# Kernel tuning notes

Measured on AMD Instinct MI355X. Metric: run time of the kernel, lower is better.

## Reference

```python
import jax, jax.numpy as jnp
import numpy as np

C_IN = 128
C_QK = C_IN // 8


def setup_inputs() -> dict:
    key = jax.random.key(0)
    kx, kq, kk, kv = jax.random.split(key, 4)
    x = jax.random.normal(kx, (8, C_IN, 64, 64), dtype=jnp.float32)
    # 1x1 conv weights, stored as (c_out, c_in); fan-in scaled init
    s = 1.0 / np.sqrt(C_IN)
    Wq = jax.random.normal(kq, (C_QK, C_IN), dtype=jnp.float32) * s
    Wk = jax.random.normal(kk, (C_QK, C_IN), dtype=jnp.float32) * s
    Wv = jax.random.normal(kv, (C_IN, C_IN), dtype=jnp.float32) * s
    gamma = jnp.ones((1,), dtype=jnp.float32) * 0.5  # nonzero so residual branch matters
    return {"x": x, "Wq": Wq, "Wk": Wk, "Wv": Wv, "gamma": gamma}


def reference(x, Wq, Wk, Wv, gamma):
    b, c, h, w = x.shape
    xt = rearr = x.reshape(b, c, h * w)            # b c n
    q = jnp.einsum('oc,bcn->bno', Wq, xt)          # b n c//8
    k = jnp.einsum('oc,bcn->bon', Wk, xt)          # b c//8 n
    v = jnp.einsum('oc,bcn->bno', Wv, xt)          # b n c
    energy = jnp.einsum('bno,bom->bnm', q, k)      # b n n (no scale, per source)
    attn = jax.nn.softmax(energy, axis=-1)
    out = jnp.einsum('bnm,bmc->bnc', attn, v)      # b n c
    out = out.transpose(0, 2, 1).reshape(b, c, h, w)
    return x + gamma[0] * out
```

## Files before the change

### kernel.cpp

```cpp
#include <hip/hip_runtime.h>
#include <hip/hip_bf16.h>


typedef __bf16 bf16x8 __attribute__((ext_vector_type(8)));
typedef __bf16 bf16x4 __attribute__((ext_vector_type(4)));
typedef float  f32x16 __attribute__((ext_vector_type(16)));

static constexpr int Bb = 8, Cc = 128, Nn = 4096, CQ = 16;

__device__ __forceinline__ f32x16 mfma32(bf16x8 a, bf16x8 b, f32x16 c) {
    return __builtin_amdgcn_mfma_f32_32x32x16_bf16(a, b, c, 0, 0, 0);
}
struct HL { __bf16 h, l; };
__device__ __forceinline__ HL hilo(float f) {
    HL r;
    r.h = (__bf16)f;
    r.l = (__bf16)(f - (float)r.h);
    return r;
}

__global__ __launch_bounds__(384) void qkv_kernel(
    const float* __restrict__ x, const float* __restrict__ Wq,
    const float* __restrict__ Wk, const float* __restrict__ Wv,
    __bf16* __restrict__ qw, __bf16* __restrict__ kw, __bf16* __restrict__ vw)
{
    const int b = blockIdx.y, tb = blockIdx.x, n0 = tb * 64, t = threadIdx.x;
    const int wave = t >> 6, lane = t & 63, lr = lane & 31, lq = lane >> 5;

    __shared__ __bf16 xh[64][136], xl[64][136];
    __shared__ __bf16 sc[4][32][40];

    if (t < 256) {
        const int n = lane, ci0 = (t >> 6) * 32;
        #pragma unroll
        for (int g = 0; g < 4; ++g) {
            float v[8];
            #pragma unroll
            for (int k = 0; k < 8; ++k)
                v[k] = x[((size_t)(b * Cc + ci0 + g * 8 + k)) * Nn + n0 + n];
            bf16x8 h8, l8;
            #pragma unroll
            for (int k = 0; k < 8; ++k) { HL z = hilo(v[k]); h8[k] = z.h; l8[k] = z.l; }
            *(bf16x8*)&xh[n][ci0 + g * 8] = h8;
            *(bf16x8*)&xl[n][ci0 + g * 8] = l8;
        }
    }
    __syncthreads();

    if (wave < 2) {
        const int nh = wave;
        const float* wrow = (lr < 16) ? (Wq + (size_t)lr * Cc)
                                      : (Wk + (size_t)(lr - 16) * Cc);
        f32x16 acc = {};
        #pragma unroll
        for (int ks = 0; ks < 8; ++ks) {
            float4 w0 = *(const float4*)(wrow + ks * 16 + lq * 8);
            float4 w1 = *(const float4*)(wrow + ks * 16 + lq * 8 + 4);
            bf16x8 ah, al;
            HL z;
            z = hilo(w0.x); ah[0] = z.h; al[0] = z.l;
            z = hilo(w0.y); ah[1] = z.h; al[1] = z.l;
            z = hilo(w0.z); ah[2] = z.h; al[2] = z.l;
            z = hilo(w0.w); ah[3] = z.h; al[3] = z.l;
            z = hilo(w1.x); ah[4] = z.h; al[4] = z.l;
            z = hilo(w1.y); ah[5] = z.h; al[5] = z.l;
            z = hilo(w1.z); ah[6] = z.h; al[6] = z.l;
            z = hilo(w1.w); ah[7] = z.h; al[7] = z.l;
            bf16x8 bh = *(const bf16x8*)&xh[nh * 32 + lr][ks * 16 + lq * 8];
            bf16x8 bl = *(const bf16x8*)&xl[nh * 32 + lr][ks * 16 + lq * 8];
            acc = mfma32(ah, bh, acc);
            acc = mfma32(al, bh, acc);
            acc = mfma32(ah, bl, acc);
        }
        const int tile = tb * 2 + nh;
        __bf16* qb = qw + (((size_t)b * 128 + tile) << 10);
        __bf16* kb = kw + (((size_t)b * 128 + tile) << 10);
        #pragma unroll
        for (int rg = 0; rg < 4; ++rg) {
            bf16x4 h4, l4;
            #pragma unroll
            for (int j = 0; j < 4; ++j) {
                float v = acc[rg * 4 + j];
                if (rg < 2) v *= 1.44269504089f;
                HL z = hilo(v);
                h4[j] = z.h; l4[j] = z.l;
            }
            const int off = (rg & 1) * 256 + lr * 8 + 4 * lq;
            __bf16* base = (rg < 2) ? qb : kb;
            *(bf16x4*)(base + off) = h4;
            *(bf16x4*)(base + 512 + off) = l4;
        }
    } else {
        const int ct = wave - 2;
        const int klr = (lr & ~12) | ((lr & 4) << 1) | ((lr & 8) >> 1);
        for (int nh = 0; nh < 2; ++nh) {
            f32x16 acc = {};
            #pragma unroll
            for (int ks = 0; ks < 8; ++ks) {
                const float* wp = Wv + (size_t)(ct * 32 + lr) * Cc + ks * 16 + lq * 8;
                float4 w0 = *(const float4*)wp;
                float4 w1 = *(const float4*)(wp + 4);
                bf16x8 a = { (__bf16)w0.x, (__bf16)w0.y, (__bf16)w0.z, (__bf16)w0.w,
                             (__bf16)w1.x, (__bf16)w1.y, (__bf16)w1.z, (__bf16)w1.w };
                bf16x8 bh = *(const bf16x8*)&xh[nh * 32 + lr][ks * 16 + lq * 8];
                acc = mfma32(a, bh, acc);
            }
            #pragma unroll
            for (int r = 0; r < 16; ++r) {
                int crow = (r & 3) + 8 * (r >> 2) + 4 * lq;
                sc[ct][crow][klr] = (__bf16)acc[r];
            }
            const int chunk = tb * 2 + nh;
            __bf16* vb = vw + (((size_t)b * 128 + chunk) << 12) + ct * 1024;
            #pragma unroll
            for (int u = 0; u < 2; ++u) {
                bf16x8 row = *(const bf16x8*)&sc[ct][lr][u * 16 + lq * 8];
                *(bf16x8*)(vb + u * 512 + lane * 8) = row;
            }
        }
    }
}

__global__ __launch_bounds__(512, 4) void attn_kernel(
    const float* __restrict__ x, const __bf16* __restrict__ qw,
    const __bf16* __restrict__ kw, const __bf16* __restrict__ vw,
    const float* __restrict__ gamma, float* __restrict__ out)
{
    const int h = blockIdx.x;
    const int b = h & 7;
    const int qt = h >> 3;
    const int t = threadIdx.x;
    const int wave = t >> 6, lane = t & 63, lr = lane & 31, lq = lane >> 5;
    const int kr = wave & 3, ch = wave >> 2;

    __shared__ float accbuf[32][129];
    __shared__ float lbuf[32];

    const __bf16* qb = qw + (((size_t)b * 128 + qt) << 10) + lane * 8;
    const bf16x8 qhi = *(const bf16x8*)qb;
    const bf16x8 qlo = *(const bf16x8*)(qb + 512);

    const int c0 = kr * 32;
    const __bf16* kp = kw + (((size_t)b * 128 + c0) << 10) + lane * 8;
    const __bf16* vp = vw + (((size_t)b * 128 + c0) << 12) + ch * 2048 + lane * 8;

    f32x16 acc0 = {}, acc1 = {};
    float l_part = 0.f;

    bf16x8 akh = *(const bf16x8*)kp,          akl = *(const bf16x8*)(kp + 512);
    bf16x8 av0 = *(const bf16x8*)vp,          av1 = *(const bf16x8*)(vp + 512);
    bf16x8 av2 = *(const bf16x8*)(vp + 1024), av3 = *(const bf16x8*)(vp + 1536);
    bf16x8 bkh, bkl, bv0, bv1, bv2, bv3;

    auto body = [&](const bf16x8& Kh, const bf16x8& Kl, const bf16x8& V0,
                    const bf16x8& V1, const bf16x8& V2, const bf16x8& V3) {
        f32x16 s = {};
        __builtin_amdgcn_s_setprio(1);
        s = mfma32(Kh, qhi, s);
        s = mfma32(Kl, qhi, s);
        s = mfma32(Kh, qlo, s);
        __builtin_amdgcn_s_setprio(0);

        float p[16];
        #pragma unroll
        for (int r = 0; r < 16; ++r) p[r] = __builtin_amdgcn_exp2f(s[r]);
        l_part += ((((p[0] + p[1]) + (p[2] + p[3])) + ((p[4] + p[5]) + (p[6] + p[7])))
                 + (((p[8] + p[9]) + (p[10] + p[11])) + ((p[12] + p[13]) + (p[14] + p[15]))));

        bf16x8 F0, F1;
        #pragma unroll
        for (int j = 0; j < 8; ++j) {
            F0[j] = (__bf16)p[j];
            F1[j] = (__bf16)p[8 + j];
        }

        __builtin_amdgcn_s_setprio(1);
        acc0 = mfma32(V0, F0, acc0);
        acc0 = mfma32(V1, F1, acc0);
        acc1 = mfma32(V2, F0, acc1);
        acc1 = mfma32(V3, F1, acc1);
        __builtin_amdgcn_s_setprio(0);
    };

    for (int it = 0; it < 15; ++it) {
        kp += 1024; vp += 4096;
        bkh = *(const bf16x8*)kp;          bkl = *(const bf16x8*)(kp + 512);
        bv0 = *(const bf16x8*)vp;          bv1 = *(const bf16x8*)(vp + 512);
        bv2 = *(const bf16x8*)(vp + 1024); bv3 = *(const bf16x8*)(vp + 1536);
        body(akh, akl, av0, av1, av2, av3);
        kp += 1024; vp += 4096;
        akh = *(const bf16x8*)kp;          akl = *(const bf16x8*)(kp + 512);
        av0 = *(const bf16x8*)vp;          av1 = *(const bf16x8*)(vp + 512);
        av2 = *(const bf16x8*)(vp + 1024); av3 = *(const bf16x8*)(vp + 1536);
        body(bkh, bkl, bv0, bv1, bv2, bv3);
    }
    kp += 1024; vp += 4096;
    bkh = *(const bf16x8*)kp;          bkl = *(const bf16x8*)(kp + 512);
    bv0 = *(const bf16x8*)vp;          bv1 = *(const bf16x8*)(vp + 512);
    bv2 = *(const bf16x8*)(vp + 1024); bv3 = *(const bf16x8*)(vp + 1536);
    body(akh, akl, av0, av1, av2, av3);
    body(bkh, bkl, bv0, bv1, bv2, bv3);

    l_part += __shfl_xor(l_part, 32);

    if (kr == 0) {
        #pragma unroll
        for (int r = 0; r < 16; ++r) {
            int c = ch * 64 + (r & 3) + 8 * (r >> 2) + 4 * lq;
            accbuf[lr][c] = acc0[r];
            accbuf[lr][c + 32] = acc1[r];
        }
        if (wave == 0 && lane < 32) lbuf[lr] = l_part;
    }
    __syncthreads();
    if (kr != 0) {
        #pragma unroll
        for (int r = 0; r < 16; ++r) {
            int c = ch * 64 + (r & 3) + 8 * (r >> 2) + 4 * lq;
            atomicAdd(&accbuf[lr][c], acc0[r]);
            atomicAdd(&accbuf[lr][c + 32], acc1[r]);
        }
        if (ch == 0 && lane < 32) atomicAdd(&lbuf[lr], l_part);
    }
    __syncthreads();

    const float g = gamma[0];
    const int q = t & 31, cg = t >> 5;
    const float linv = 1.0f / lbuf[q];
    const int n0b = qt * 32;
    #pragma unroll
    for (int i = 0; i < 8; ++i) {
        int c = cg + 16 * i;
        size_t idx = ((size_t)(b * Cc + c)) * Nn + n0b + q;
        out[idx] = x[idx] + g * accbuf[q][c] * linv;
    }
}

extern "C" void kernel_launch(void* const* d_in, const int* in_sizes, int n_in,
                              void* d_out, int out_size, void* d_ws, size_t ws_size,
                              hipStream_t stream) {
    const float* x  = (const float*)d_in[0];
    const float* Wq = (const float*)d_in[1];
    const float* Wk = (const float*)d_in[2];
    const float* Wv = (const float*)d_in[3];
    const float* gm = (const float*)d_in[4];

    __bf16* qw = (__bf16*)d_ws;
    __bf16* kw = qw + (size_t)Bb * 128 * 1024;
    __bf16* vw = kw + (size_t)Bb * 128 * 1024;

    qkv_kernel<<<dim3(Nn / 64, Bb), 384, 0, stream>>>(x, Wq, Wk, Wv, qw, kw, vw);
    attn_kernel<<<dim3(Nn / 32 * Bb), 512, 0, stream>>>(x, qw, kw, vw, gm,
                                                        (float*)d_out);
}
```

Before: 188.9 us.

## Have each attention wave compute all 128 output channels, halving the block size

The attention kernel drops from 8 waves (4 key-range groups × 2 channel halves) to 4 waves, and each wave now accumulates all 128 output channels in four accumulators. The QK^T energy MFMAs and exp2 softmax work were previously duplicated across the two channel-half waves and are now computed once per key tile. The cost is more VGPRs per wave (8 V fragments double-buffered plus 4 accumulators), fewer waves to hide latency, and launch bounds changed to 256 threads with min 2 blocks.

```diff
diff --git a/kernel.cpp b/kernel.cpp
--- a/kernel.cpp
+++ b/kernel.cpp
@@ -121,7 +121,7 @@
     }
 }
 
-__global__ __launch_bounds__(512, 4) void attn_kernel(
+__global__ __launch_bounds__(256, 2) void attn_kernel(
     const float* __restrict__ x, const __bf16* __restrict__ qw,
     const __bf16* __restrict__ kw, const __bf16* __restrict__ vw,
     const float* __restrict__ gamma, float* __restrict__ out)
@@ -131,7 +131,7 @@
     const int qt = h >> 3;
     const int t = threadIdx.x;
     const int wave = t >> 6, lane = t & 63, lr = lane & 31, lq = lane >> 5;
-    const int kr = wave & 3, ch = wave >> 2;
+    const int kr = wave;
 
     __shared__ float accbuf[32][129];
     __shared__ float lbuf[32];
@@ -142,18 +142,18 @@
 
     const int c0 = kr * 32;
     const __bf16* kp = kw + (((size_t)b * 128 + c0) << 10) + lane * 8;
-    const __bf16* vp = vw + (((size_t)b * 128 + c0) << 12) + ch * 2048 + lane * 8;
-
-    f32x16 acc0 = {}, acc1 = {};
+    const __bf16* vp = vw + (((size_t)b * 128 + c0) << 12) + lane * 8;
+
+    f32x16 acc[4] = {{}, {}, {}, {}};
     float l_part = 0.f;
 
-    bf16x8 akh = *(const bf16x8*)kp,          akl = *(const bf16x8*)(kp + 512);
-    bf16x8 av0 = *(const bf16x8*)vp,          av1 = *(const bf16x8*)(vp + 512);
-    bf16x8 av2 = *(const bf16x8*)(vp + 1024), av3 = *(const bf16x8*)(vp + 1536);
-    bf16x8 bkh, bkl, bv0, bv1, bv2, bv3;
-
-    auto body = [&](const bf16x8& Kh, const bf16x8& Kl, const bf16x8& V0,
-                    const bf16x8& V1, const bf16x8& V2, const bf16x8& V3) {
+    bf16x8 akh = *(const bf16x8*)kp, akl = *(const bf16x8*)(kp + 512);
+    bf16x8 av[8], bv[8];
+    #pragma unroll
+    for (int u = 0; u < 8; ++u) av[u] = *(const bf16x8*)(vp + u * 512);
+    bf16x8 bkh, bkl;
+
+    auto body = [&](const bf16x8& Kh, const bf16x8& Kl, const bf16x8 (&V)[8]) {
         f32x16 s = {};
         __builtin_amdgcn_s_setprio(1);
         s = mfma32(Kh, qhi, s);
@@ -175,52 +175,55 @@
         }
 
         __builtin_amdgcn_s_setprio(1);
-        acc0 = mfma32(V0, F0, acc0);
-        acc0 = mfma32(V1, F1, acc0);
-        acc1 = mfma32(V2, F0, acc1);
-        acc1 = mfma32(V3, F1, acc1);
+        #pragma unroll
+        for (int ct = 0; ct < 4; ++ct) {
+            acc[ct] = mfma32(V[2 * ct],     F0, acc[ct]);
+            acc[ct] = mfma32(V[2 * ct + 1], F1, acc[ct]);
+        }
         __builtin_amdgcn_s_setprio(0);
     };
 
     for (int it = 0; it < 15; ++it) {
         kp += 1024; vp += 4096;
-        bkh = *(const bf16x8*)kp;          bkl = *(const bf16x8*)(kp + 512);
-        bv0 = *(const bf16x8*)vp;          bv1 = *(const bf16x8*)(vp + 512);
-        bv2 = *(const bf16x8*)(vp + 1024); bv3 = *(const bf16x8*)(vp + 1536);
-        body(akh, akl, av0, av1, av2, av3);
+        bkh = *(const bf16x8*)kp; bkl = *(const bf16x8*)(kp + 512);
+        #pragma unroll
+        for (int u = 0; u < 8; ++u) bv[u] = *(const bf16x8*)(vp + u * 512);
+        body(akh, akl, av);
         kp += 1024; vp += 4096;
-        akh = *(const bf16x8*)kp;          akl = *(const bf16x8*)(kp + 512);
-        av0 = *(const bf16x8*)vp;          av1 = *(const bf16x8*)(vp + 512);
-        av2 = *(const bf16x8*)(vp + 1024); av3 = *(const bf16x8*)(vp + 1536);
-        body(bkh, bkl, bv0, bv1, bv2, bv3);
+        akh = *(const bf16x8*)kp; akl = *(const bf16x8*)(kp + 512);
+        #pragma unroll
+        for (int u = 0; u < 8; ++u) av[u] = *(const bf16x8*)(vp + u * 512);
+        body(bkh, bkl, bv);
     }
     kp += 1024; vp += 4096;
-    bkh = *(const bf16x8*)kp;          bkl = *(const bf16x8*)(kp + 512);
-    bv0 = *(const bf16x8*)vp;          bv1 = *(const bf16x8*)(vp + 512);
-    bv2 = *(const bf16x8*)(vp + 1024); bv3 = *(const bf16x8*)(vp + 1536);
-    body(akh, akl, av0, av1, av2, av3);
-    body(bkh, bkl, bv0, bv1, bv2, bv3);
+    bkh = *(const bf16x8*)kp; bkl = *(const bf16x8*)(kp + 512);
+    #pragma unroll
+    for (int u = 0; u < 8; ++u) bv[u] = *(const bf16x8*)(vp + u * 512);
+    body(akh, akl, av);
+    body(bkh, bkl, bv);
 
     l_part += __shfl_xor(l_part, 32);
 
     if (kr == 0) {
         #pragma unroll
-        for (int r = 0; r < 16; ++r) {
-            int c = ch * 64 + (r & 3) + 8 * (r >> 2) + 4 * lq;
-            accbuf[lr][c] = acc0[r];
-            accbuf[lr][c + 32] = acc1[r];
-        }
-        if (wave == 0 && lane < 32) lbuf[lr] = l_part;
+        for (int ct = 0; ct < 4; ++ct)
+            #pragma unroll
+            for (int r = 0; r < 16; ++r) {
+                int c = (r & 3) + 8 * (r >> 2) + 4 * lq + 32 * ct;
+                accbuf[lr][c] = acc[ct][r];
+            }
+        if (lane < 32) lbuf[lr] = l_part;
     }
     __syncthreads();
     if (kr != 0) {
         #pragma unroll
-        for (int r = 0; r < 16; ++r) {
-            int c = ch * 64 + (r & 3) + 8 * (r >> 2) + 4 * lq;
-            atomicAdd(&accbuf[lr][c], acc0[r]);
-            atomicAdd(&accbuf[lr][c + 32], acc1[r]);
-        }
-        if (ch == 0 && lane < 32) atomicAdd(&lbuf[lr], l_part);
+        for (int ct = 0; ct < 4; ++ct)
+            #pragma unroll
+            for (int r = 0; r < 16; ++r) {
+                int c = (r & 3) + 8 * (r >> 2) + 4 * lq + 32 * ct;
+                atomicAdd(&accbuf[lr][c], acc[ct][r]);
+            }
+        if (lane < 32) atomicAdd(&lbuf[lr], l_part);
     }
     __syncthreads();
 
@@ -229,8 +232,8 @@
     const float linv = 1.0f / lbuf[q];
     const int n0b = qt * 32;
     #pragma unroll
-    for (int i = 0; i < 8; ++i) {
-        int c = cg + 16 * i;
+    for (int i = 0; i < 16; ++i) {
+        int c = cg + 8 * i;
         size_t idx = ((size_t)(b * Cc + c)) * Nn + n0b + q;
         out[idx] = x[idx] + g * accbuf[q][c] * linv;
     }
@@ -250,6 +253,6 @@
     __bf16* vw = kw + (size_t)Bb * 128 * 1024;
 
     qkv_kernel<<<dim3(Nn / 64, Bb), 384, 0, stream>>>(x, Wq, Wk, Wv, qw, kw, vw);
-    attn_kernel<<<dim3(Nn / 32 * Bb), 512, 0, stream>>>(x, qw, kw, vw, gm,
+    attn_kernel<<<dim3(Nn / 32 * Bb), 256, 0, stream>>>(x, qw, kw, vw, gm,
                                                         (float*)d_out);
 }
```

New measurement: 187.4 us. No clear change (-0.8%).
